# Kernel tuning notes

Hardware: AMD Instinct MI355X
Metric: run time of the kernel (lower is better)

Reference implementation:

```python
import jax, jax.numpy as jnp
import numpy as np

N, C, H, W = 512, 64, 32, 32
HID, HEADS = 128, 4
E = 16384
BN_EPS = 1e-5


def conv2d(x, w, b, pad):
    y = jax.lax.conv_general_dilated(x, w, (1, 1), [(pad, pad), (pad, pad)],
                                     dimension_numbers=('NCHW', 'OIHW', 'NCHW'))
    return y + b[None, :, None, None]


def bn_eval(x, g, b):
    # inference BN with running_mean=0, running_var=1
    scale = g * (1.0 / np.sqrt(1.0 + BN_EPS))
    return x * scale[None, :, None, None] + b[None, :, None, None]


def gat_layer(x, src, dst, lin_w, att_s, att_d, bias):
    # x: (N, in) -> (N, HID); PyG GATConv heads=4, concat=False, add_self_loops
    h = (x @ lin_w).reshape(N, HEADS, HID)          # (N, H, D)
    a_s = jnp.einsum('nhd,hd->nh', h, att_s)        # source score
    a_d = jnp.einsum('nhd,hd->nh', h, att_d)        # target score
    e = jax.nn.leaky_relu(a_s[src] + a_d[dst], 0.2)  # (E', H)
    m = jax.ops.segment_max(e, dst, num_segments=N)
    ex = jnp.exp(e - m[dst])
    denom = jax.ops.segment_sum(ex, dst, num_segments=N)
    alpha = ex / (denom[dst] + 1e-16)               # per-target softmax
    out = jax.ops.segment_sum(alpha[:, :, None] * h[src], dst, num_segments=N)
    return out.mean(axis=1) + bias                  # concat=False -> head mean


def setup_inputs() -> dict:
    key = jax.random.key(0)
    ks = jax.random.split(key, 24)
    s = lambda *shape: 0.05
    d = {}
    d['x'] = jax.random.normal(ks[0], (N, C, H, W), jnp.float32)
    d['edge_index'] = jax.random.randint(ks[1], (2, E), 0, N, jnp.int64)
    d['confidence_maps'] = jax.random.uniform(ks[2], (N, 1, H, W), jnp.float32)
    # feature encoder: 1x1 conv + BN
    d['fe_w'] = jax.random.normal(ks[3], (HID, C, 1, 1), jnp.float32) * 0.05
    d['fe_b'] = jnp.zeros((HID,), jnp.float32)
    d['fe_g'] = jnp.ones((HID,), jnp.float32)
    d['fe_beta'] = jnp.zeros((HID,), jnp.float32)
    # spatial processor: two 3x3 conv + BN
    d['sp_w1'] = jax.random.normal(ks[4], (HID, HID, 3, 3), jnp.float32) * 0.02
    d['sp_b1'] = jnp.zeros((HID,), jnp.float32)
    d['sp_g1'] = jnp.ones((HID,), jnp.float32)
    d['sp_be1'] = jnp.zeros((HID,), jnp.float32)
    d['sp_w2'] = jax.random.normal(ks[5], (HID, HID, 3, 3), jnp.float32) * 0.02
    d['sp_b2'] = jnp.zeros((HID,), jnp.float32)
    d['sp_g2'] = jnp.ones((HID,), jnp.float32)
    d['sp_be2'] = jnp.zeros((HID,), jnp.float32)
    # GAT layers (in=HID, out=HID, heads=HEADS)
    d['g1_lin'] = jax.random.normal(ks[6], (HID, HEADS * HID), jnp.float32) * 0.05
    d['g1_as'] = jax.random.normal(ks[7], (HEADS, HID), jnp.float32) * 0.05
    d['g1_ad'] = jax.random.normal(ks[8], (HEADS, HID), jnp.float32) * 0.05
    d['g1_b'] = jnp.zeros((HID,), jnp.float32)
    d['g2_lin'] = jax.random.normal(ks[9], (HID, HEADS * HID), jnp.float32) * 0.05
    d['g2_as'] = jax.random.normal(ks[10], (HEADS, HID), jnp.float32) * 0.05
    d['g2_ad'] = jax.random.normal(ks[11], (HEADS, HID), jnp.float32) * 0.05
    d['g2_b'] = jnp.zeros((HID,), jnp.float32)
    # output projector 1x1 conv
    d['op_w'] = jax.random.normal(ks[12], (C, HID, 1, 1), jnp.float32) * 0.05
    d['op_b'] = jnp.zeros((C,), jnp.float32)
    return d


def reference(x, edge_index, confidence_maps, fe_w, fe_b, fe_g, fe_beta,
              sp_w1, sp_b1, sp_g1, sp_be1, sp_w2, sp_b2, sp_g2, sp_be2,
              g1_lin, g1_as, g1_ad, g1_b, g2_lin, g2_as, g2_ad, g2_b,
              op_w, op_b):
    # feature encoder + confidence modulation
    xe = jax.nn.relu(bn_eval(conv2d(x, fe_w, fe_b, 0), fe_g, fe_beta))
    xe = xe * confidence_maps
    # spatial processor
    xp = jax.nn.relu(bn_eval(conv2d(xe, sp_w1, sp_b1, 1), sp_g1, sp_be1))
    xp = jax.nn.relu(bn_eval(conv2d(xp, sp_w2, sp_b2, 1), sp_g2, sp_be2))
    # global avg pool -> node features (N, HID)
    x_node = xp.mean(axis=(2, 3))
    # add self loops once
    sl = jnp.arange(N, dtype=edge_index.dtype)
    src = jnp.concatenate([edge_index[0], sl])
    dst = jnp.concatenate([edge_index[1], sl])
    xg = jax.nn.relu(gat_layer(x_node, src, dst, g1_lin, g1_as, g1_ad, g1_b))
    xg = jax.nn.relu(gat_layer(xg, src, dst, g2_lin, g2_as, g2_ad, g2_b))
    # broadcast-add GNN output back onto spatial maps
    x_comb = xg[:, :, None, None] + xp
    return conv2d(x_comb, op_w, op_b, 0)
```

## Files before the change

kernel.cpp:

```cpp
#include <hip/hip_runtime.h>
#include <stdint.h>

#define NIMG 512
#define CINCH 64
#define HIDC 128
#define NEDGE 16384
#define HWPIX 1024
#define PW2 34
#define PPIX 1156

typedef __attribute__((ext_vector_type(8))) short bf16x8;
typedef __attribute__((ext_vector_type(4))) float f32x4;
typedef __attribute__((ext_vector_type(16))) float f32x16;

static __device__ __forceinline__ unsigned short f2bf(float f){
  unsigned u = __builtin_bit_cast(unsigned, f);
  u += 0x7FFFu + ((u>>16)&1u);
  return (unsigned short)(u>>16);
}
static __device__ __forceinline__ float bf2f(unsigned short s){
  unsigned u = ((unsigned)s)<<16;
  return __builtin_bit_cast(float, u);
}

static __device__ __forceinline__ void gload16(const char* src, char* dst){
  __builtin_amdgcn_global_load_lds(
      (const __attribute__((address_space(1))) unsigned int*)src,
      (__attribute__((address_space(3))) unsigned int*)dst, 16, 0, 0);
}

__global__ void k_init(unsigned short* xe_pad, unsigned short* xp1_pad,
                       float* xnode_acc, int* cnt, int* pos){
  int idx = blockIdx.x*256 + threadIdx.x;
  int total_b = NIMG*132*16;
  for(int i = idx; i < total_b; i += gridDim.x*256){
    int img = i / (132*16);
    int rem = i - img*(132*16);
    int bp = rem >> 4;
    int slot = rem & 15;
    int r, c;
    if(bp < 34){ r = 0; c = bp; }
    else if(bp < 68){ r = 33; c = bp-34; }
    else if(bp < 100){ r = bp-68+1; c = 0; }
    else { r = bp-100+1; c = 33; }
    size_t off = ((size_t)img*PPIX + r*PW2 + c)*128 + slot*8;
    uint4 z = {0,0,0,0};
    *(uint4*)(xe_pad + off) = z;
    *(uint4*)(xp1_pad + off) = z;
  }
  for(int i = idx; i < NIMG*HIDC; i += gridDim.x*256) xnode_acc[i] = 0.f;
  for(int i = idx; i < NIMG; i += gridDim.x*256){ cnt[i] = 0; pos[i] = 0; }
}

__global__ void k_wconv(const float* __restrict__ sp_w1, const float* __restrict__ sp_w2,
                        const float* __restrict__ fe_w, const float* __restrict__ op_w,
                        unsigned short* Wb1, unsigned short* Wb2,
                        unsigned short* Wfe, unsigned short* Wop){
  int idx = blockIdx.x*256 + threadIdx.x;
  for(int i = idx; i < 147456; i += gridDim.x*256){
    int j = i & 7, cc = (i>>3)&15, co = (i>>7)&127, tap = i>>14;
    int cin = ((cc ^ (co&7))<<3) + j;
    Wb1[i] = f2bf(sp_w1[(co*128+cin)*9 + tap]);
    Wb2[i] = f2bf(sp_w2[(co*128+cin)*9 + tap]);
  }
  for(int i = idx; i < 8192; i += gridDim.x*256){
    int j = i & 7, s = (i>>3)&7, co = i>>6;
    int ci = ((s ^ (co&7))<<3) + j;
    Wfe[i] = f2bf(fe_w[co*64+ci]);
  }
  for(int i = idx; i < 8192; i += gridDim.x*256){
    int j = i & 7, s = (i>>3)&15, co = i>>7;
    int cin = ((s ^ (co&7))<<3) + j;
    Wop[i] = f2bf(op_w[co*128+cin]);
  }
}

__global__ void k_csr_count(const int* __restrict__ ei, int* cnt){
  int e = blockIdx.x*256 + threadIdx.x;
  if(e < NEDGE) atomicAdd(&cnt[ei[NEDGE+e]], 1);
}
__global__ void k_csr_scan(const int* __restrict__ cnt, int* offs){
  __shared__ int sc[512];
  int t = threadIdx.x;
  sc[t] = cnt[t] + 1;
  __syncthreads();
  for(int o = 1; o < 512; o <<= 1){
    int add = (t >= o) ? sc[t-o] : 0;
    __syncthreads();
    sc[t] += add;
    __syncthreads();
  }
  if(t == 0) offs[0] = 0;
  offs[t+1] = sc[t];
}
__global__ void k_csr_fill(const int* __restrict__ ei, const int* __restrict__ offs,
                           int* pos, int* csr_src){
  int e = blockIdx.x*256 + threadIdx.x;
  if(e < NEDGE + NIMG){
    int s, d;
    if(e < NEDGE){ s = ei[e]; d = ei[NEDGE+e]; }
    else { s = e - NEDGE; d = s; }
    int slot = offs[d] + atomicAdd(&pos[d], 1);
    csr_src[slot] = s;
  }
}

__launch_bounds__(256, 2)
__global__ void k_encode(const float* __restrict__ x, const float* __restrict__ conf,
                         const unsigned short* __restrict__ Wfe,
                         const float* __restrict__ fe_b, const float* __restrict__ fe_g,
                         const float* __restrict__ fe_beta,
                         unsigned short* __restrict__ xe_pad){
  __shared__ char lds[49152];
  char* xa = lds; char* wb = lds + 32768;
  int tid = threadIdx.x;
  int n = blockIdx.x >> 3, rg = blockIdx.x & 7;
  int hw0 = rg*128;
  {
    int q = tid >> 3, c0 = tid & 7;
    const float* xb = x + (size_t)n*CINCH*HWPIX + hw0;
    #pragma unroll
    for(int cc = 0; cc < 8; ++cc){
      int c = cc*8 + c0;
      float4 v = *(const float4*)(xb + (size_t)c*HWPIX + q*4);
      float vv[4] = {v.x, v.y, v.z, v.w};
      #pragma unroll
      for(int i = 0; i < 4; ++i){
        int p = q*4 + i;
        *(float*)(xa + p*256 + ((cc ^ (p&7))*32) + c0*4) = vv[i];
      }
    }
    #pragma unroll
    for(int it = 0; it < 4; ++it){
      uint4 w = *(const uint4*)((const char*)Wfe + it*4096 + tid*16);
      *(uint4*)(wb + it*4096 + tid*16) = w;
    }
  }
  __syncthreads();
  int wid = tid>>6, lane = tid&63;
  int wr = wid>>1, wc = wid&1, fr = lane&15, fq = lane>>4;
  f32x4 acc[4][4];
  #pragma unroll
  for(int a = 0; a < 4; ++a)
    #pragma unroll
    for(int b = 0; b < 4; ++b) acc[a][b] = (f32x4){0.f,0.f,0.f,0.f};
  #pragma unroll
  for(int kc = 0; kc < 2; ++kc){
    bf16x8 af[4], bfr[4];
    #pragma unroll
    for(int mi = 0; mi < 4; ++mi){
      int p = wr*64 + mi*16 + fr;
      int u = kc*4 + fq;
      const float* src = (const float*)(xa + p*256 + ((u ^ (p&7))*32));
      float4 lo = *(const float4*)src;
      float4 hi = *(const float4*)(src+4);
      bf16x8 a;
      a[0]=(short)f2bf(lo.x); a[1]=(short)f2bf(lo.y); a[2]=(short)f2bf(lo.z); a[3]=(short)f2bf(lo.w);
      a[4]=(short)f2bf(hi.x); a[5]=(short)f2bf(hi.y); a[6]=(short)f2bf(hi.z); a[7]=(short)f2bf(hi.w);
      af[mi] = a;
    }
    #pragma unroll
    for(int nf = 0; nf < 4; ++nf){
      int co = wc*64 + nf*16 + fr;
      int slot = (kc*4 + fq) ^ (co&7);
      bfr[nf] = *(const bf16x8*)(wb + co*128 + slot*16);
    }
    #pragma unroll
    for(int mi = 0; mi < 4; ++mi)
      #pragma unroll
      for(int nf = 0; nf < 4; ++nf)
        acc[mi][nf] = __builtin_amdgcn_mfma_f32_16x16x32_bf16(af[mi], bfr[nf], acc[mi][nf], 0,0,0);
  }
  __syncthreads();
  {
    const float rs = 0.9999950000374997f;
    float kb[4], ks[4], kbe[4];
    #pragma unroll
    for(int nf = 0; nf < 4; ++nf){
      int co = wc*64 + nf*16 + fr;
      kb[nf] = fe_b[co]; ks[nf] = fe_g[co]*rs; kbe[nf] = fe_beta[co];
    }
    #pragma unroll
    for(int mi = 0; mi < 4; ++mi)
      #pragma unroll
      for(int j = 0; j < 4; ++j){
        int px = wr*64 + mi*16 + fq*4 + j;
        float cf = conf[(size_t)n*HWPIX + hw0 + px];
        #pragma unroll
        for(int nf = 0; nf < 4; ++nf){
          float v = (acc[mi][nf][j] + kb[nf])*ks[nf] + kbe[nf];
          v = fmaxf(v, 0.f)*cf;
          int co = wc*64 + nf*16 + fr;
          *(unsigned short*)(xa + px*256 + ((co*2) ^ (((px>>2)&7)<<4))) = f2bf(v);
        }
      }
  }
  __syncthreads();
  {
    int p = tid>>1, half = tid&1;
    int r = rg*4 + (p>>5), c = p&31;
    int key = (2*(p>>5) + (p&31) + 3) & 7;
    unsigned short* dst = xe_pad + ((size_t)n*PPIX + (r+1)*PW2 + (c+1))*128;
    #pragma unroll
    for(int s = 0; s < 8; ++s){
      int ls = half*8 + s;
      uint4 v = *(uint4*)(xa + p*256 + ((ls*16) ^ (((p>>2)&7)<<4)));
      *(uint4*)(dst + (ls ^ key)*8) = v;
    }
  }
}

__launch_bounds__(512, 2)
__global__ void k_conv3(const unsigned short* __restrict__ inp,
                        const unsigned short* __restrict__ Wb,
                        const float* __restrict__ bnb, const float* __restrict__ bng,
                        const float* __restrict__ bnbe,
                        unsigned short* __restrict__ outp,
                        float* __restrict__ xnode_acc, int mode){
  extern __shared__ char lds[];
  char* Ab = lds;
  char* Wd = lds + 87040;
  int tid = threadIdx.x;
  int n = blockIdx.x>>2, rg = blockIdx.x&3;

  const char* img  = (const char*)inp + ((size_t)n*PPIX + (size_t)rg*8*PW2)*256;
  const char* wsrc = (const char*)Wb;

  #pragma unroll
  for(int it = 0; it < 4; ++it)
    gload16(wsrc + it*8192 + tid*16, Wd + it*8192 + tid*16);
  #pragma unroll
  for(int it = 0; it < 11; ++it){
    int j = tid + it*512;
    if(it < 10 || j < 5440) gload16(img + (size_t)j*16, Ab + (size_t)j*16);
  }

  int wid = tid>>6, lane = tid&63;
  int wr = wid>>1, wc = wid&1;
  int col = lane&31, hi = lane>>5;
  int cobase0 = (wc*64 + col)*256;
  int cokeyx = col&7;

  f32x16 acc[2][2];
  #pragma unroll
  for(int a = 0; a < 2; ++a)
    #pragma unroll
    for(int b = 0; b < 2; ++b)
      #pragma unroll
      for(int r = 0; r < 16; ++r) acc[a][b][r] = 0.f;

  __syncthreads();

  for(int tap = 0; tap < 9; ++tap){
    if(tap < 8){
      const char* ws = wsrc + (size_t)(tap+1)*32768;
      char* wdst = Wd + ((tap+1)&1)*32768;
      #pragma unroll
      for(int it = 0; it < 4; ++it)
        gload16(ws + it*8192 + tid*16, wdst + it*8192 + tid*16);
    }
    const char* cur = Wd + (tap&1)*32768;
    int dy = tap/3 - 1, dx = tap - (tap/3)*3 - 1;
    int pcol = col + 1 + dx;
    int prow0 = wr*2 + 1 + dy;
    int abase0 = prow0*8704 + pcol*256;
    int key0 = (2*prow0 + pcol) & 7;
    int key1 = (key0 + 2) & 7;

    __builtin_amdgcn_s_setprio(1);
    #pragma unroll
    for(int kc = 0; kc < 8; ++kc){
      int g = kc*2 + hi;
      bf16x8 af0 = *(const bf16x8*)(Ab + abase0 + ((g ^ key0)<<4));
      bf16x8 af1 = *(const bf16x8*)(Ab + abase0 + 8704 + ((g ^ key1)<<4));
      int wco = (g ^ cokeyx)<<4;
      bf16x8 wf0 = *(const bf16x8*)(cur + cobase0 + wco);
      bf16x8 wf1 = *(const bf16x8*)(cur + cobase0 + 8192 + wco);
      acc[0][0] = __builtin_amdgcn_mfma_f32_32x32x16_bf16(af0, wf0, acc[0][0], 0,0,0);
      acc[0][1] = __builtin_amdgcn_mfma_f32_32x32x16_bf16(af0, wf1, acc[0][1], 0,0,0);
      acc[1][0] = __builtin_amdgcn_mfma_f32_32x32x16_bf16(af1, wf0, acc[1][0], 0,0,0);
      acc[1][1] = __builtin_amdgcn_mfma_f32_32x32x16_bf16(af1, wf1, acc[1][1], 0,0,0);
    }
    __builtin_amdgcn_s_setprio(0);
    __syncthreads();
  }

  char* eb = Ab;
  {
    const float rs = 0.9999950000374997f;
    float kb[2], ks[2], kbe[2];
    #pragma unroll
    for(int nf = 0; nf < 2; ++nf){
      int co = wc*64 + nf*32 + col;
      kb[nf] = bnb[co]; ks[nf] = bng[co]*rs; kbe[nf] = bnbe[co];
    }
    #pragma unroll
    for(int mi = 0; mi < 2; ++mi)
      #pragma unroll
      for(int reg = 0; reg < 16; ++reg){
        int pc = (reg&3) + 8*(reg>>2) + 4*hi;
        int px = (wr*2 + mi)*32 + pc;
        #pragma unroll
        for(int nf = 0; nf < 2; ++nf){
          float v = (acc[mi][nf][reg] + kb[nf])*ks[nf] + kbe[nf];
          v = fmaxf(v, 0.f);
          int co = wc*64 + nf*32 + col;
          *(unsigned short*)(eb + px*256 + ((co*2) ^ (((px>>2)&7)<<4))) = f2bf(v);
        }
      }
  }
  __syncthreads();
  {
    int p = tid>>1, half = tid&1;
    int r = rg*8 + (p>>5), c = p&31;
    unsigned short* dst;
    int key;
    if(mode == 0){
      key = (2*(p>>5) + (p&31) + 3) & 7;
      dst = outp + ((size_t)n*PPIX + (r+1)*PW2 + (c+1))*128;
    } else {
      key = p & 7;
      dst = outp + ((size_t)n*HWPIX + rg*256 + p)*128;
    }
    #pragma unroll
    for(int s = 0; s < 8; ++s){
      int ls = half*8 + s;
      uint4 v = *(uint4*)(eb + p*256 + ((ls*16) ^ (((p>>2)&7)<<4)));
      *(uint4*)(dst + (ls ^ key)*8) = v;
    }
  }
  if(mode == 1){
    int co = tid & 127, g = tid>>7;
    float sum = 0.f;
    #pragma unroll 8
    for(int i = 0; i < 64; ++i){
      int px = g*64 + i;
      sum += bf2f(*(unsigned short*)(eb + px*256 + ((co*2) ^ (((px>>2)&7)<<4))));
    }
    atomicAdd(&xnode_acc[n*HIDC + co], sum);
  }
}

__global__ void k_gat_lin(const float* __restrict__ xin, float scale,
                          const float* __restrict__ lin,
                          const float* __restrict__ as_, const float* __restrict__ ad_,
                          float* __restrict__ h, float* __restrict__ a_s, float* __restrict__ a_d){
  __shared__ float xs[128];
  __shared__ float rs0[4], rs1[4], rd0[4], rd1[4];
  int n = blockIdx.x, t = threadIdx.x;
  if(t < 128) xs[t] = xin[n*128 + t]*scale;
  __syncthreads();
  float o0 = 0.f, o1 = 0.f;
  for(int k = 0; k < 128; ++k){
    float xv = xs[k];
    o0 += xv*lin[k*512 + t];
    o1 += xv*lin[k*512 + t + 256];
  }
  h[(size_t)n*512 + t] = o0;
  h[(size_t)n*512 + t + 256] = o1;
  float s0 = o0*as_[t], s1 = o1*as_[t+256];
  float d0 = o0*ad_[t], d1 = o1*ad_[t+256];
  #pragma unroll
  for(int o = 32; o; o >>= 1){
    s0 += __shfl_down(s0, o); s1 += __shfl_down(s1, o);
    d0 += __shfl_down(d0, o); d1 += __shfl_down(d1, o);
  }
  int w = t>>6;
  if((t&63) == 0){ rs0[w]=s0; rs1[w]=s1; rd0[w]=d0; rd1[w]=d1; }
  __syncthreads();
  if(t < 4){
    if(t < 2){
      a_s[n*4+t] = rs0[2*t] + rs0[2*t+1];
      a_d[n*4+t] = rd0[2*t] + rd0[2*t+1];
    } else {
      a_s[n*4+t] = rs1[2*(t-2)] + rs1[2*(t-2)+1];
      a_d[n*4+t] = rd1[2*(t-2)] + rd1[2*(t-2)+1];
    }
  }
}

__global__ void k_gat_aggr(const int* __restrict__ offs, const int* __restrict__ csr_src,
                           const float* __restrict__ a_s, const float* __restrict__ a_d,
                           const float* __restrict__ h, const float* __restrict__ bias,
                           float* __restrict__ y){
  __shared__ int ssrc[2048];
  __shared__ float sex[4][2048];
  __shared__ float out4[512];
  __shared__ float adn[4], smax[4], sden[4];
  __shared__ float wred[4][4];
  int n = blockIdx.x, t = threadIdx.x;
  int base = offs[n], deg = offs[n+1] - base;
  if(t < 4) adn[t] = a_d[n*4 + t];
  __syncthreads();
  bool cached = (deg <= 2048);
  float lm0=-1e30f, lm1=-1e30f, lm2=-1e30f, lm3=-1e30f;
  for(int e = t; e < deg; e += 256){
    int s = csr_src[base + e];
    float v0 = a_s[s*4+0] + adn[0]; v0 = v0 > 0.f ? v0 : 0.2f*v0;
    float v1 = a_s[s*4+1] + adn[1]; v1 = v1 > 0.f ? v1 : 0.2f*v1;
    float v2 = a_s[s*4+2] + adn[2]; v2 = v2 > 0.f ? v2 : 0.2f*v2;
    float v3 = a_s[s*4+3] + adn[3]; v3 = v3 > 0.f ? v3 : 0.2f*v3;
    if(cached){ ssrc[e]=s; sex[0][e]=v0; sex[1][e]=v1; sex[2][e]=v2; sex[3][e]=v3; }
    lm0 = fmaxf(lm0, v0); lm1 = fmaxf(lm1, v1); lm2 = fmaxf(lm2, v2); lm3 = fmaxf(lm3, v3);
  }
  #pragma unroll
  for(int o = 32; o; o >>= 1){
    lm0 = fmaxf(lm0, __shfl_down(lm0, o)); lm1 = fmaxf(lm1, __shfl_down(lm1, o));
    lm2 = fmaxf(lm2, __shfl_down(lm2, o)); lm3 = fmaxf(lm3, __shfl_down(lm3, o));
  }
  int w = t>>6;
  if((t&63) == 0){ wred[w][0]=lm0; wred[w][1]=lm1; wred[w][2]=lm2; wred[w][3]=lm3; }
  __syncthreads();
  if(t < 4) smax[t] = fmaxf(fmaxf(wred[0][t], wred[1][t]), fmaxf(wred[2][t], wred[3][t]));
  __syncthreads();
  float m0 = smax[0], m1 = smax[1], m2 = smax[2], m3 = smax[3];
  float ls0=0.f, ls1=0.f, ls2=0.f, ls3=0.f;
  for(int e = t; e < deg; e += 256){
    float e0, e1, e2, e3;
    if(cached){ e0 = sex[0][e]; e1 = sex[1][e]; e2 = sex[2][e]; e3 = sex[3][e]; }
    else {
      int s = csr_src[base + e];
      e0 = a_s[s*4+0] + adn[0]; e0 = e0 > 0.f ? e0 : 0.2f*e0;
      e1 = a_s[s*4+1] + adn[1]; e1 = e1 > 0.f ? e1 : 0.2f*e1;
      e2 = a_s[s*4+2] + adn[2]; e2 = e2 > 0.f ? e2 : 0.2f*e2;
      e3 = a_s[s*4+3] + adn[3]; e3 = e3 > 0.f ? e3 : 0.2f*e3;
    }
    e0 = __expf(e0-m0); e1 = __expf(e1-m1); e2 = __expf(e2-m2); e3 = __expf(e3-m3);
    if(cached){ sex[0][e]=e0; sex[1][e]=e1; sex[2][e]=e2; sex[3][e]=e3; }
    ls0 += e0; ls1 += e1; ls2 += e2; ls3 += e3;
  }
  #pragma unroll
  for(int o = 32; o; o >>= 1){
    ls0 += __shfl_down(ls0, o); ls1 += __shfl_down(ls1, o);
    ls2 += __shfl_down(ls2, o); ls3 += __shfl_down(ls3, o);
  }
  __syncthreads();
  if((t&63) == 0){ wred[w][0]=ls0; wred[w][1]=ls1; wred[w][2]=ls2; wred[w][3]=ls3; }
  __syncthreads();
  if(t < 4) sden[t] = wred[0][t] + wred[1][t] + wred[2][t] + wred[3][t] + 1e-16f;
  __syncthreads();
  #pragma unroll
  for(int oo = 0; oo < 2; ++oo){
    int o = t + oo*256;
    int hd = o>>7, d = o&127;
    float mh = smax[hd];
    float accv = 0.f;
    for(int e = 0; e < deg; ++e){
      float ex; int s;
      if(cached){ ex = sex[hd][e]; s = ssrc[e]; }
      else {
        s = csr_src[base + e];
        float v = a_s[s*4+hd] + adn[hd]; v = v > 0.f ? v : 0.2f*v;
        ex = __expf(v - mh);
      }
      accv += ex * h[(size_t)s*512 + hd*128 + d];
    }
    out4[o] = accv / sden[hd];
  }
  __syncthreads();
  if(t < 128){
    float v = (out4[t] + out4[128+t] + out4[256+t] + out4[384+t])*0.25f + bias[t];
    y[n*128 + t] = fmaxf(v, 0.f);
  }
}

__global__ void k_nodebias(const float* __restrict__ xg2, const float* __restrict__ op_w,
                           const float* __restrict__ op_b, float* __restrict__ nb){
  int g = blockIdx.x*256 + threadIdx.x;
  if(g < NIMG*64){
    int n = g>>6, co = g&63;
    float acc = op_b[co];
    for(int k = 0; k < 128; ++k) acc += op_w[co*128+k]*xg2[n*128+k];
    nb[g] = acc;
  }
}

__launch_bounds__(256, 2)
__global__ void k_outconv(const unsigned short* __restrict__ xp2,
                          const unsigned short* __restrict__ Wop,
                          const float* __restrict__ nb, float* __restrict__ out){
  __shared__ char lds[16384];
  int tid = threadIdx.x;
  int n = blockIdx.x>>3, rg = blockIdx.x&7;
  #pragma unroll
  for(int it = 0; it < 4; ++it){
    uint4 v = *(const uint4*)((const char*)Wop + it*4096 + tid*16);
    *(uint4*)(lds + it*4096 + tid*16) = v;
  }
  __syncthreads();
  int wid = tid>>6, lane = tid&63;
  int wr = wid>>1, wc = wid&1, fr = lane&15, fq = lane>>4;
  f32x4 acc[4][2];
  #pragma unroll
  for(int a = 0; a < 4; ++a){ acc[a][0] = (f32x4){0.f,0.f,0.f,0.f}; acc[a][1] = (f32x4){0.f,0.f,0.f,0.f}; }
  const unsigned short* abase = xp2 + ((size_t)n*HWPIX + rg*128)*128;
  #pragma unroll
  for(int kc = 0; kc < 4; ++kc){
    bf16x8 af[4], bfr[2];
    #pragma unroll
    for(int mi = 0; mi < 4; ++mi){
      int p = wr*64 + mi*16 + fr;
      af[mi] = *(const bf16x8*)(abase + p*128 + (((kc*4+fq) ^ (p&7))*8));
    }
    #pragma unroll
    for(int nf = 0; nf < 2; ++nf){
      int co = wc*32 + nf*16 + fr;
      int slot = (kc*4 + fq) ^ (co&7);
      bfr[nf] = *(const bf16x8*)(lds + co*256 + slot*16);
    }
    #pragma unroll
    for(int mi = 0; mi < 4; ++mi)
      #pragma unroll
      for(int nf = 0; nf < 2; ++nf)
        acc[mi][nf] = __builtin_amdgcn_mfma_f32_16x16x32_bf16(af[mi], bfr[nf], acc[mi][nf], 0,0,0);
  }
  #pragma unroll
  for(int mi = 0; mi < 4; ++mi)
    #pragma unroll
    for(int nf = 0; nf < 2; ++nf){
      int co = wc*32 + nf*16 + fr;
      int hw = rg*128 + wr*64 + mi*16 + fq*4;
      float nbv = nb[n*64 + co];
      float4 v = { acc[mi][nf][0]+nbv, acc[mi][nf][1]+nbv, acc[mi][nf][2]+nbv, acc[mi][nf][3]+nbv };
      *(float4*)(out + ((size_t)n*64 + co)*HWPIX + hw) = v;
    }
}

extern "C" void kernel_launch(void* const* d_in, const int* in_sizes, int n_in,
                              void* d_out, int out_size, void* d_ws, size_t ws_size,
                              hipStream_t stream){
  const float* x       = (const float*)d_in[0];
  const int*   ei      = (const int*)d_in[1];
  const float* conf    = (const float*)d_in[2];
  const float* fe_w    = (const float*)d_in[3];
  const float* fe_b    = (const float*)d_in[4];
  const float* fe_g    = (const float*)d_in[5];
  const float* fe_beta = (const float*)d_in[6];
  const float* sp_w1   = (const float*)d_in[7];
  const float* sp_b1   = (const float*)d_in[8];
  const float* sp_g1   = (const float*)d_in[9];
  const float* sp_be1  = (const float*)d_in[10];
  const float* sp_w2   = (const float*)d_in[11];
  const float* sp_b2   = (const float*)d_in[12];
  const float* sp_g2   = (const float*)d_in[13];
  const float* sp_be2  = (const float*)d_in[14];
  const float* g1_lin  = (const float*)d_in[15];
  const float* g1_as   = (const float*)d_in[16];
  const float* g1_ad   = (const float*)d_in[17];
  const float* g1_b    = (const float*)d_in[18];
  const float* g2_lin  = (const float*)d_in[19];
  const float* g2_as   = (const float*)d_in[20];
  const float* g2_ad   = (const float*)d_in[21];
  const float* g2_b    = (const float*)d_in[22];
  const float* op_w    = (const float*)d_in[23];
  const float* op_b    = (const float*)d_in[24];
  float* out = (float*)d_out;

  char* ws = (char*)d_ws;
  size_t off = 0;
  auto alloc = [&](size_t bytes)->char*{
    char* p = ws + off; off += (bytes + 255) & ~(size_t)255; return p;
  };
  unsigned short* bigA  = (unsigned short*)alloc((size_t)NIMG*PPIX*128*2);
  unsigned short* xp1   = (unsigned short*)alloc((size_t)NIMG*PPIX*128*2);
  unsigned short* Wb1   = (unsigned short*)alloc(147456*2);
  unsigned short* Wb2   = (unsigned short*)alloc(147456*2);
  unsigned short* Wfe   = (unsigned short*)alloc(8192*2);
  unsigned short* Wop   = (unsigned short*)alloc(8192*2);
  float* xnode_acc = (float*)alloc(NIMG*HIDC*4);
  float* h     = (float*)alloc((size_t)NIMG*512*4);
  float* a_s   = (float*)alloc(NIMG*4*4);
  float* a_d   = (float*)alloc(NIMG*4*4);
  float* xg1   = (float*)alloc(NIMG*HIDC*4);
  float* xg2   = (float*)alloc(NIMG*HIDC*4);
  int* cnt     = (int*)alloc(NIMG*4);
  int* pos     = (int*)alloc(NIMG*4);
  int* offs    = (int*)alloc((NIMG+1)*4);
  int* csr_src = (int*)alloc((NEDGE+NIMG)*4);
  float* nb    = (float*)alloc(NIMG*64*4);
  if(off > ws_size) return;
  unsigned short* xp2 = bigA;

  hipFuncSetAttribute((const void*)k_conv3,
                      hipFuncAttributeMaxDynamicSharedMemorySize, 152576);

  k_init<<<1024, 256, 0, stream>>>(bigA, xp1, xnode_acc, cnt, pos);
  k_wconv<<<576, 256, 0, stream>>>(sp_w1, sp_w2, fe_w, op_w, Wb1, Wb2, Wfe, Wop);
  k_csr_count<<<(NEDGE+255)/256, 256, 0, stream>>>(ei, cnt);
  k_csr_scan<<<1, 512, 0, stream>>>(cnt, offs);
  k_csr_fill<<<(NEDGE+NIMG+255)/256, 256, 0, stream>>>(ei, offs, pos, csr_src);
  k_encode<<<4096, 256, 0, stream>>>(x, conf, Wfe, fe_b, fe_g, fe_beta, bigA);
  k_conv3<<<2048, 512, 152576, stream>>>(bigA, Wb1, sp_b1, sp_g1, sp_be1, xp1, xnode_acc, 0);
  k_conv3<<<2048, 512, 152576, stream>>>(xp1, Wb2, sp_b2, sp_g2, sp_be2, xp2, xnode_acc, 1);
  k_gat_lin<<<512, 256, 0, stream>>>(xnode_acc, 1.f/1024.f, g1_lin, g1_as, g1_ad, h, a_s, a_d);
  k_gat_aggr<<<512, 256, 0, stream>>>(offs, csr_src, a_s, a_d, h, g1_b, xg1);
  k_gat_lin<<<512, 256, 0, stream>>>(xg1, 1.f, g2_lin, g2_as, g2_ad, h, a_s, a_d);
  k_gat_aggr<<<512, 256, 0, stream>>>(offs, csr_src, a_s, a_d, h, g2_b, xg2);
  k_nodebias<<<(NIMG*64+255)/256, 256, 0, stream>>>(xg2, op_w, op_b, nb);
  k_outconv<<<4096, 256, 0, stream>>>(xp2, Wop, nb, out);
}
```

Baseline: 597.6 us.

## Pad conv3 LDS rows and switch to additive rotation swizzle; fuse node pooling

```diff
diff --git a/kernel.cpp b/kernel.cpp
--- a/kernel.cpp
+++ b/kernel.cpp
@@ -8,6 +8,8 @@
 #define HWPIX 1024
 #define PW2 34
 #define PPIX 1156
+#define APITCH 272
+#define AROW 9248
 
 typedef __attribute__((ext_vector_type(8))) short bf16x8;
 typedef __attribute__((ext_vector_type(4))) float f32x4;
@@ -58,8 +60,8 @@
                         unsigned short* Wfe, unsigned short* Wop){
   int idx = blockIdx.x*256 + threadIdx.x;
   for(int i = idx; i < 147456; i += gridDim.x*256){
-    int j = i & 7, cc = (i>>3)&15, co = (i>>7)&127, tap = i>>14;
-    int cin = ((cc ^ (co&7))<<3) + j;
+    int j = i & 7, slot = (i>>3)&15, co = (i>>7)&127, tap = i>>14;
+    int cin = (((slot - 3*co) & 15)<<3) + j;
     Wb1[i] = f2bf(sp_w1[(co*128+cin)*9 + tap]);
     Wb2[i] = f2bf(sp_w2[(co*128+cin)*9 + tap]);
   }
@@ -199,13 +201,13 @@
   {
     int p = tid>>1, half = tid&1;
     int r = rg*4 + (p>>5), c = p&31;
-    int key = (2*(p>>5) + (p&31) + 3) & 7;
+    int key = 2*((p&31) + 1);
     unsigned short* dst = xe_pad + ((size_t)n*PPIX + (r+1)*PW2 + (c+1))*128;
     #pragma unroll
     for(int s = 0; s < 8; ++s){
       int ls = half*8 + s;
       uint4 v = *(uint4*)(xa + p*256 + ((ls*16) ^ (((p>>2)&7)<<4)));
-      *(uint4*)(dst + (ls ^ key)*8) = v;
+      *(uint4*)(dst + ((ls + key)&15)*8) = v;
     }
   }
 }
@@ -219,7 +221,7 @@
                         float* __restrict__ xnode_acc, int mode){
   extern __shared__ char lds[];
   char* Ab = lds;
-  char* Wd = lds + 87040;
+  char* Wd = lds + 93184;
   int tid = threadIdx.x;
   int n = blockIdx.x>>2, rg = blockIdx.x&3;
 
@@ -230,16 +232,20 @@
   for(int it = 0; it < 4; ++it)
     gload16(wsrc + it*8192 + tid*16, Wd + it*8192 + tid*16);
   #pragma unroll
-  for(int it = 0; it < 11; ++it){
+  for(int it = 0; it < 12; ++it){
     int j = tid + it*512;
-    if(it < 10 || j < 5440) gload16(img + (size_t)j*16, Ab + (size_t)j*16);
+    if(it < 11 || j < 5824){
+      int pidx = j/17, s = j - pidx*17;
+      if(pidx > 339) pidx = 339;
+      if(s == 16) s = 0;
+      gload16(img + (size_t)pidx*256 + s*16, Ab + (size_t)j*16);
+    }
   }
 
   int wid = tid>>6, lane = tid&63;
   int wr = wid>>1, wc = wid&1;
   int col = lane&31, hi = lane>>5;
-  int cobase0 = (wc*64 + col)*256;
-  int cokeyx = col&7;
+  int cob = (wc*64 + col)*256;
 
   f32x16 acc[2][2];
   #pragma unroll
@@ -263,19 +269,18 @@
     int dy = tap/3 - 1, dx = tap - (tap/3)*3 - 1;
     int pcol = col + 1 + dx;
     int prow0 = wr*2 + 1 + dy;
-    int abase0 = prow0*8704 + pcol*256;
-    int key0 = (2*prow0 + pcol) & 7;
-    int key1 = (key0 + 2) & 7;
-
+    int a0 = prow0*AROW + pcol*APITCH;
+    int ka = 2*pcol;
     __builtin_amdgcn_s_setprio(1);
     #pragma unroll
     for(int kc = 0; kc < 8; ++kc){
       int g = kc*2 + hi;
-      bf16x8 af0 = *(const bf16x8*)(Ab + abase0 + ((g ^ key0)<<4));
-      bf16x8 af1 = *(const bf16x8*)(Ab + abase0 + 8704 + ((g ^ key1)<<4));
-      int wco = (g ^ cokeyx)<<4;
-      bf16x8 wf0 = *(const bf16x8*)(cur + cobase0 + wco);
-      bf16x8 wf1 = *(const bf16x8*)(cur + cobase0 + 8192 + wco);
+      int sa = ((g + ka)&15)<<4;
+      bf16x8 af0 = *(const bf16x8*)(Ab + a0 + sa);
+      bf16x8 af1 = *(const bf16x8*)(Ab + a0 + AROW + sa);
+      int sw = ((g + 3*col)&15)<<4;
+      bf16x8 wf0 = *(const bf16x8*)(cur + cob + sw);
+      bf16x8 wf1 = *(const bf16x8*)(cur + cob + 8192 + sw);
       acc[0][0] = __builtin_amdgcn_mfma_f32_32x32x16_bf16(af0, wf0, acc[0][0], 0,0,0);
       acc[0][1] = __builtin_amdgcn_mfma_f32_32x32x16_bf16(af0, wf1, acc[0][1], 0,0,0);
       acc[1][0] = __builtin_amdgcn_mfma_f32_32x32x16_bf16(af1, wf0, acc[1][0], 0,0,0);
@@ -286,6 +291,7 @@
   }
 
   char* eb = Ab;
+  float sn0 = 0.f, sn1 = 0.f;
   {
     const float rs = 0.9999950000374997f;
     float kb[2], ks[2], kbe[2];
@@ -304,10 +310,19 @@
         for(int nf = 0; nf < 2; ++nf){
           float v = (acc[mi][nf][reg] + kb[nf])*ks[nf] + kbe[nf];
           v = fmaxf(v, 0.f);
+          if(nf == 0) sn0 += v; else sn1 += v;
           int co = wc*64 + nf*32 + col;
           *(unsigned short*)(eb + px*256 + ((co*2) ^ (((px>>2)&7)<<4))) = f2bf(v);
         }
       }
+  }
+  if(mode == 1){
+    sn0 += __shfl_down(sn0, 32);
+    sn1 += __shfl_down(sn1, 32);
+    if(lane < 32){
+      atomicAdd(&xnode_acc[n*HIDC + wc*64 + col], sn0);
+      atomicAdd(&xnode_acc[n*HIDC + wc*64 + 32 + col], sn1);
+    }
   }
   __syncthreads();
   {
@@ -316,28 +331,18 @@
     unsigned short* dst;
     int key;
     if(mode == 0){
-      key = (2*(p>>5) + (p&31) + 3) & 7;
+      key = 2*((p&31) + 1);
       dst = outp + ((size_t)n*PPIX + (r+1)*PW2 + (c+1))*128;
     } else {
-      key = p & 7;
+      key = 3*p;
       dst = outp + ((size_t)n*HWPIX + rg*256 + p)*128;
     }
     #pragma unroll
     for(int s = 0; s < 8; ++s){
       int ls = half*8 + s;
       uint4 v = *(uint4*)(eb + p*256 + ((ls*16) ^ (((p>>2)&7)<<4)));
-      *(uint4*)(dst + (ls ^ key)*8) = v;
-    }
-  }
-  if(mode == 1){
-    int co = tid & 127, g = tid>>7;
-    float sum = 0.f;
-    #pragma unroll 8
-    for(int i = 0; i < 64; ++i){
-      int px = g*64 + i;
-      sum += bf2f(*(unsigned short*)(eb + px*256 + ((co*2) ^ (((px>>2)&7)<<4))));
-    }
-    atomicAdd(&xnode_acc[n*HIDC + co], sum);
+      *(uint4*)(dst + ((ls + key)&15)*8) = v;
+    }
   }
 }
 
@@ -500,7 +505,7 @@
     #pragma unroll
     for(int mi = 0; mi < 4; ++mi){
       int p = wr*64 + mi*16 + fr;
-      af[mi] = *(const bf16x8*)(abase + p*128 + (((kc*4+fq) ^ (p&7))*8));
+      af[mi] = *(const bf16x8*)(abase + p*128 + (((kc*4+fq) + 3*p)&15)*8);
     }
     #pragma unroll
     for(int nf = 0; nf < 2; ++nf){
@@ -582,7 +587,7 @@
   unsigned short* xp2 = bigA;
 
   hipFuncSetAttribute((const void*)k_conv3,
-                      hipFuncAttributeMaxDynamicSharedMemorySize, 152576);
+                      hipFuncAttributeMaxDynamicSharedMemorySize, 158720);
 
   k_init<<<1024, 256, 0, stream>>>(bigA, xp1, xnode_acc, cnt, pos);
   k_wconv<<<576, 256, 0, stream>>>(sp_w1, sp_w2, fe_w, op_w, Wb1, Wb2, Wfe, Wop);
@@ -590,8 +595,8 @@
   k_csr_scan<<<1, 512, 0, stream>>>(cnt, offs);
   k_csr_fill<<<(NEDGE+NIMG+255)/256, 256, 0, stream>>>(ei, offs, pos, csr_src);
   k_encode<<<4096, 256, 0, stream>>>(x, conf, Wfe, fe_b, fe_g, fe_beta, bigA);
-  k_conv3<<<2048, 512, 152576, stream>>>(bigA, Wb1, sp_b1, sp_g1, sp_be1, xp1, xnode_acc, 0);
-  k_conv3<<<2048, 512, 152576, stream>>>(xp1, Wb2, sp_b2, sp_g2, sp_be2, xp2, xnode_acc, 1);
+  k_conv3<<<2048, 512, 158720, stream>>>(bigA, Wb1, sp_b1, sp_g1, sp_be1, xp1, xnode_acc, 0);
+  k_conv3<<<2048, 512, 158720, stream>>>(xp1, Wb2, sp_b2, sp_g2, sp_be2, xp2, xnode_acc, 1);
   k_gat_lin<<<512, 256, 0, stream>>>(xnode_acc, 1.f/1024.f, g1_lin, g1_as, g1_ad, h, a_s, a_d);
   k_gat_aggr<<<512, 256, 0, stream>>>(offs, csr_src, a_s, a_d, h, g1_b, xg1);
   k_gat_lin<<<512, 256, 0, stream>>>(xg1, 1.f, g2_lin, g2_as, g2_ad, h, a_s, a_d);
```

Result: no change. 604.4 us (+1.1%).
